# Kernel tuning notes

Measured on AMD Instinct MI355X. Metric: run time of the kernel, lower is better.

## Reference

```python
import jax, jax.numpy as jnp
import numpy as np

N_NODES = 100000
N_EDGES = 3200000
D_FEAT = 256
HIDDEN = 16


def setup_inputs() -> dict:
    key = jax.random.key(0)
    k1, k2, k3, k4 = jax.random.split(key, 4)
    x = jax.random.normal(k1, (N_NODES, D_FEAT), dtype=jnp.float32)
    edge_index = jax.random.randint(k2, (2, N_EDGES), 0, N_NODES, dtype=jnp.int64)
    # GCNConv linear weight (Glorot-ish scale) and bias
    W = jax.random.normal(k3, (D_FEAT, HIDDEN), dtype=jnp.float32) / np.sqrt(D_FEAT)
    b_conv = jnp.zeros((HIDDEN,), dtype=jnp.float32)
    W_fc = jax.random.normal(k4, (HIDDEN, 1), dtype=jnp.float32) / np.sqrt(HIDDEN)
    b_fc = jnp.zeros((1,), dtype=jnp.float32)
    return {"x": x, "edge_index": edge_index, "W": W, "b_conv": b_conv,
            "W_fc": W_fc, "b_fc": b_fc}


def reference(x, edge_index, W, b_conv, W_fc, b_fc):
    N = x.shape[0]
    # --- GCNConv: add self-loops, symmetric normalization, transform, scatter-add ---
    loop = jnp.arange(N, dtype=edge_index.dtype)
    src = jnp.concatenate([edge_index[0], loop])  # message sources (x_j)
    dst = jnp.concatenate([edge_index[1], loop])  # aggregation targets
    # degree of target nodes (edge weights = 1, self-loops included)
    deg = jax.ops.segment_sum(jnp.ones_like(dst, dtype=x.dtype), dst, num_segments=N)
    dinv = jnp.where(deg > 0, jax.lax.rsqrt(deg), 0.0)
    norm = dinv[src] * dinv[dst]  # [E+N]
    h = x @ W                       # [N, hidden] transform before propagation
    msg = h[src] * norm[:, None]    # gather + scale
    agg = jax.ops.segment_sum(msg, dst, num_segments=N)  # scatter-add
    out = agg + b_conv
    return out @ W_fc + b_fc
```

## Files before the change

kernel.cpp:

```cpp
#include <hip/hip_runtime.h>

#define DF 256
#define HID 16
#define WB 1024
#define PBITS 8
#define PMAX 512

__global__ void __launch_bounds__(256)
hist_kernel(const int* __restrict__ dst, unsigned* __restrict__ cntT, int P, int E, int Epw) {
    __shared__ unsigned h[PMAX];
    for (int i = threadIdx.x; i < P; i += 256) h[i] = 0u;
    __syncthreads();
    const int w = blockIdx.x;
    const size_t e0 = (size_t)w * Epw;
    long rem = (long)E - (long)e0;
    int m = rem < 0 ? 0 : (rem > Epw ? Epw : (int)rem);
    int i = threadIdx.x;
    for (; i + 768 < m; i += 1024) {
        unsigned d0 = (unsigned)dst[e0 + i];
        unsigned d1 = (unsigned)dst[e0 + i + 256];
        unsigned d2 = (unsigned)dst[e0 + i + 512];
        unsigned d3 = (unsigned)dst[e0 + i + 768];
        atomicAdd(&h[d0 >> PBITS], 1u); atomicAdd(&h[d1 >> PBITS], 1u);
        atomicAdd(&h[d2 >> PBITS], 1u); atomicAdd(&h[d3 >> PBITS], 1u);
    }
    for (; i < m; i += 256) atomicAdd(&h[((unsigned)dst[e0 + i]) >> PBITS], 1u);
    __syncthreads();
    for (int p = threadIdx.x; p < P; p += 256) cntT[(size_t)p * WB + w] = h[p];
}

__global__ void __launch_bounds__(1024)
rowscan_kernel(unsigned* __restrict__ cntT, unsigned* __restrict__ rowTotal) {
    __shared__ unsigned wsum[16];
    const int p = blockIdx.x, t = threadIdx.x, lane = t & 63, wv = t >> 6;
    unsigned v = cntT[(size_t)p * WB + t];
    unsigned xi = v;
#pragma unroll
    for (int off = 1; off < 64; off <<= 1) {
        unsigned u = __shfl_up(xi, off, 64);
        if (lane >= off) xi += u;
    }
    if (lane == 63) wsum[wv] = xi;
    __syncthreads();
    if (t < 16) {
        unsigned u = wsum[t];
#pragma unroll
        for (int off = 1; off < 16; off <<= 1) {
            unsigned uu = __shfl_up(u, off, 64);
            if (t >= off) u += uu;
        }
        wsum[t] = u;
    }
    __syncthreads();
    unsigned base = wv ? wsum[wv - 1] : 0u;
    cntT[(size_t)p * WB + t] = xi - v + base;
    if (t == 1023) rowTotal[p] = xi + base;
}

__global__ void __launch_bounds__(512)
partscan_kernel(const unsigned* __restrict__ rowTotal, unsigned* __restrict__ partBase,
                int P, int E) {
    __shared__ unsigned wsum[8];
    const int t = threadIdx.x, lane = t & 63, wv = t >> 6;
    unsigned v = (t < P) ? rowTotal[t] : 0u;
    unsigned xi = v;
#pragma unroll
    for (int off = 1; off < 64; off <<= 1) {
        unsigned u = __shfl_up(xi, off, 64);
        if (lane >= off) xi += u;
    }
    if (lane == 63) wsum[wv] = xi;
    __syncthreads();
    if (t < 8) {
        unsigned u = wsum[t];
#pragma unroll
        for (int off = 1; off < 8; off <<= 1) {
            unsigned uu = __shfl_up(u, off, 64);
            if (t >= off) u += uu;
        }
        wsum[t] = u;
    }
    __syncthreads();
    unsigned base = wv ? wsum[wv - 1] : 0u;
    if (t < P) partBase[t] = xi - v + base;
    if (t == 0) partBase[P] = (unsigned)E;
}

__global__ void __launch_bounds__(512)
binscatter_kernel(const int* __restrict__ src, const int* __restrict__ dst,
                  const unsigned* __restrict__ cntT, const unsigned* __restrict__ partBase,
                  unsigned* __restrict__ sorted, int P, int E, int Epw) {
    __shared__ unsigned cur[PMAX];
    const int w = blockIdx.x;
    for (int p = threadIdx.x; p < P; p += 512)
        cur[p] = partBase[p] + cntT[(size_t)p * WB + w];
    __syncthreads();
    const size_t e0 = (size_t)w * Epw;
    long rem = (long)E - (long)e0;
    int m = rem < 0 ? 0 : (rem > Epw ? Epw : (int)rem);
    int i = threadIdx.x;
    for (; i + 1536 < m; i += 2048) {
        unsigned s0 = (unsigned)src[e0 + i],        d0 = (unsigned)dst[e0 + i];
        unsigned s1 = (unsigned)src[e0 + i + 512],  d1 = (unsigned)dst[e0 + i + 512];
        unsigned s2 = (unsigned)src[e0 + i + 1024], d2 = (unsigned)dst[e0 + i + 1024];
        unsigned s3 = (unsigned)src[e0 + i + 1536], d3 = (unsigned)dst[e0 + i + 1536];
        unsigned t0 = atomicAdd(&cur[d0 >> PBITS], 1u);
        unsigned t1 = atomicAdd(&cur[d1 >> PBITS], 1u);
        unsigned t2 = atomicAdd(&cur[d2 >> PBITS], 1u);
        unsigned t3 = atomicAdd(&cur[d3 >> PBITS], 1u);
        sorted[t0] = (s0 << PBITS) | (d0 & 255u);
        sorted[t1] = (s1 << PBITS) | (d1 & 255u);
        sorted[t2] = (s2 << PBITS) | (d2 & 255u);
        sorted[t3] = (s3 << PBITS) | (d3 & 255u);
    }
    for (; i < m; i += 512) {
        unsigned s = (unsigned)src[e0 + i], d = (unsigned)dst[e0 + i];
        unsigned slot = atomicAdd(&cur[d >> PBITS], 1u);
        sorted[slot] = (s << PBITS) | (d & 255u);
    }
}

__global__ void __launch_bounds__(1024)
degfin_sval_kernel(const float* __restrict__ x, const unsigned* __restrict__ sorted,
                   const unsigned* __restrict__ partBase, const float* __restrict__ Wm,
                   const float* __restrict__ W_fc, float* __restrict__ dinv,
                   float* __restrict__ tval, int N) {
    __shared__ unsigned dc[256];
    __shared__ float sly[256];
    const int p = blockIdx.x, t = threadIdx.x;
    if (t < 256) dc[t] = 0u;
    __syncthreads();
    const unsigned b0 = partBase[p], b1 = partBase[p + 1];
    unsigned j = b0 + t;
    for (; j + 3072 < b1; j += 4096) {
        unsigned e0 = sorted[j], e1 = sorted[j + 1024], e2 = sorted[j + 2048], e3 = sorted[j + 3072];
        atomicAdd(&dc[e0 & 255u], 1u); atomicAdd(&dc[e1 & 255u], 1u);
        atomicAdd(&dc[e2 & 255u], 1u); atomicAdd(&dc[e3 & 255u], 1u);
    }
    for (; j < b1; j += 1024) atomicAdd(&dc[sorted[j] & 255u], 1u);
    {
        const int lane = t & 63, wv = t >> 6;
        float a0 = 0.f, a1 = 0.f, a2 = 0.f, a3 = 0.f;
        const float* wrow = Wm + (size_t)(lane * 4) * HID;
#pragma unroll
        for (int k = 0; k < HID; ++k) {
            float f = W_fc[k];
            a0 += wrow[k] * f;
            a1 += wrow[HID + k] * f;
            a2 += wrow[2 * HID + k] * f;
            a3 += wrow[3 * HID + k] * f;
        }
        for (int k = 0; k < 8; ++k) {
            int ra = wv + 16 * k, rb = ra + 128;
            int ia = (p << PBITS) + ra, ib = (p << PBITS) + rb;
            float sa = 0.f, sb = 0.f;
            if (ia < N) {
                float4 xa = reinterpret_cast<const float4*>(x + (size_t)ia * DF)[lane];
                sa = xa.x * a0 + xa.y * a1 + xa.z * a2 + xa.w * a3;
            }
            if (ib < N) {
                float4 xb = reinterpret_cast<const float4*>(x + (size_t)ib * DF)[lane];
                sb = xb.x * a0 + xb.y * a1 + xb.z * a2 + xb.w * a3;
            }
#pragma unroll
            for (int off = 32; off > 0; off >>= 1) {
                sa += __shfl_xor(sa, off, 64);
                sb += __shfl_xor(sb, off, 64);
            }
            if (lane == 0) { sly[ra] = sa; sly[rb] = sb; }
        }
    }
    __syncthreads();
    if (t < 256) {
        int i = (p << PBITS) + t;
        if (i < N) {
            float deg = 1.0f + (float)dc[t];
            float di = rsqrtf(deg);
            dinv[i] = di;
            tval[i] = sly[t] * di;
        }
    }
}

__global__ void __launch_bounds__(1024)
reduce_kernel(const unsigned* __restrict__ sorted, const unsigned* __restrict__ partBase,
              const float* __restrict__ tval, const float* __restrict__ dinv,
              const float* __restrict__ b_conv, const float* __restrict__ W_fc,
              const float* __restrict__ b_fc, float* __restrict__ out, int N) {
    __shared__ float facc[256];
    const int p = blockIdx.x, t = threadIdx.x;
    if (t < 256) facc[t] = 0.f;
    __syncthreads();
    const unsigned b0 = partBase[p], b1 = partBase[p + 1];
    unsigned j = b0 + t;
    for (; j + 3072 < b1; j += 4096) {
        unsigned e0 = sorted[j], e1 = sorted[j + 1024], e2 = sorted[j + 2048], e3 = sorted[j + 3072];
        float v0 = tval[e0 >> PBITS], v1 = tval[e1 >> PBITS];
        float v2 = tval[e2 >> PBITS], v3 = tval[e3 >> PBITS];
        atomicAdd(&facc[e0 & 255u], v0); atomicAdd(&facc[e1 & 255u], v1);
        atomicAdd(&facc[e2 & 255u], v2); atomicAdd(&facc[e3 & 255u], v3);
    }
    for (; j < b1; j += 1024) {
        unsigned e = sorted[j];
        atomicAdd(&facc[e & 255u], tval[e >> PBITS]);
    }
    __syncthreads();
    if (t < 256) {
        int i = (p << PBITS) + t;
        if (i < N) {
            float c = 0.f;
#pragma unroll
            for (int k = 0; k < HID; ++k) c += b_conv[k] * W_fc[k];
            float di = dinv[i];
            out[i] = di * (tval[i] + facc[t]) + c + b_fc[0];
        }
    }
}

__global__ void fb_sval(const float* __restrict__ x, const float* __restrict__ Wm,
                        const float* __restrict__ W_fc, float* __restrict__ sv, int N) {
    __shared__ float wl[DF];
    int k = threadIdx.x;
    float a = 0.f;
#pragma unroll
    for (int j = 0; j < HID; ++j) a += Wm[k * HID + j] * W_fc[j];
    wl[k] = a;
    __syncthreads();
    int lane = threadIdx.x & 63, wid = threadIdx.x >> 6;
    float4 wv = reinterpret_cast<const float4*>(wl)[lane];
    for (int row = blockIdx.x * 4 + wid; row < N; row += gridDim.x * 4) {
        float4 xv = reinterpret_cast<const float4*>(x + (size_t)row * DF)[lane];
        float acc = xv.x * wv.x + xv.y * wv.y + xv.z * wv.z + xv.w * wv.w;
#pragma unroll
        for (int off = 32; off > 0; off >>= 1) acc += __shfl_xor(acc, off, 64);
        if (lane == 0) sv[row] = acc;
    }
}
__global__ void fb_count(const int* __restrict__ dst, unsigned* __restrict__ cnt, int E) {
    int stride = gridDim.x * blockDim.x;
    for (int e = blockIdx.x * blockDim.x + threadIdx.x; e < E; e += stride)
        atomicAdd(&cnt[dst[e]], 1u);
}
__global__ void fb_node(const unsigned* __restrict__ cnt, const float* __restrict__ sv,
                        const float* __restrict__ b_conv, const float* __restrict__ W_fc,
                        const float* __restrict__ b_fc, float* __restrict__ dinv,
                        float* __restrict__ tval, float* __restrict__ out, int N) {
    int i = blockIdx.x * blockDim.x + threadIdx.x;
    if (i < N) {
        float c = 0.f;
#pragma unroll
        for (int j = 0; j < HID; ++j) c += b_conv[j] * W_fc[j];
        float deg = 1.0f + (float)cnt[i];
        float di = rsqrtf(deg);
        float s = sv[i];
        dinv[i] = di; tval[i] = s * di;
        out[i] = s / deg + c + b_fc[0];
    }
}
__global__ void fb_scatter(const int* __restrict__ src, const int* __restrict__ dst,
                           const float* __restrict__ tval, const float* __restrict__ dinv,
                           float* __restrict__ out, int E) {
    int stride = gridDim.x * blockDim.x;
    for (int e = blockIdx.x * blockDim.x + threadIdx.x; e < E; e += stride) {
        int si = src[e], di = dst[e];
        atomicAdd(&out[di], tval[si] * dinv[di]);
    }
}

extern "C" void kernel_launch(void* const* d_in, const int* in_sizes, int n_in,
                              void* d_out, int out_size, void* d_ws, size_t ws_size,
                              hipStream_t stream) {
    const float* x      = (const float*)d_in[0];
    const int*   ei     = (const int*)d_in[1];
    const float* Wm     = (const float*)d_in[2];
    const float* b_conv = (const float*)d_in[3];
    const float* W_fc   = (const float*)d_in[4];
    const float* b_fc   = (const float*)d_in[5];
    float* out = (float*)d_out;

    const int N = in_sizes[0] / DF;
    const int E = in_sizes[1] / 2;
    const int* src = ei;
    const int* dst = ei + E;

    const int P   = (N + 255) >> PBITS;
    const int Epw = (E + WB - 1) / WB;

    char* ws = (char*)d_ws;
    float* dinv = (float*)ws;
    float* tval = dinv + N;
    unsigned* cntT     = (unsigned*)(tval + N);
    unsigned* rowTotal = cntT + (size_t)P * WB;
    unsigned* partBase = rowTotal + 512;
    unsigned* sorted   = partBase + 520;

    const size_t need = ((size_t)2 * N + (size_t)P * WB + 512 + 520 + (size_t)E) * 4;

    if (P >= 1 && P <= PMAX && N <= (1 << 23) && ws_size >= need) {
        hist_kernel<<<WB, 256, 0, stream>>>(dst, cntT, P, E, Epw);
        rowscan_kernel<<<P, 1024, 0, stream>>>(cntT, rowTotal);
        partscan_kernel<<<1, 512, 0, stream>>>(rowTotal, partBase, P, E);
        binscatter_kernel<<<WB, 512, 0, stream>>>(src, dst, cntT, partBase, sorted, P, E, Epw);
        degfin_sval_kernel<<<P, 1024, 0, stream>>>(x, sorted, partBase, Wm, W_fc, dinv, tval, N);
        reduce_kernel<<<P, 1024, 0, stream>>>(sorted, partBase, tval, dinv,
                                              b_conv, W_fc, b_fc, out, N);
    } else {
        float* sv = tval + N;
        unsigned* fcnt = (unsigned*)(sv + N);
        hipMemsetAsync(fcnt, 0, (size_t)N * 4, stream);
        fb_sval<<<2048, 256, 0, stream>>>(x, Wm, W_fc, sv, N);
        fb_count<<<2048, 256, 0, stream>>>(dst, fcnt, E);
        fb_node<<<(N + 255) / 256, 256, 0, stream>>>(fcnt, sv, b_conv, W_fc, b_fc, dinv, tval, out, N);
        fb_scatter<<<2048, 256, 0, stream>>>(src, dst, tval, dinv, out, E);
    }
}
```

Baseline: 101.0 us.

## Fuse x-projection into histogram kernel and halve edge-chunk block count

Moves the per-node projection of x onto W·W_fc out of the degree-finalize kernel and into the histogram kernel, which processes rows in a grid-stride loop with four rows in flight per wave. The histogram block count drops from 1024 to 512 with 512 threads each, and the count matrix is stored block-major with padding, so the row scan now reads it strided. The aim is to overlap the large x read with the light histogram pass and to spread it across the whole grid instead of one block per partition. The cost is an extra N-float buffer for sv and a strided access pattern in the scan.

```diff
diff --git a/kernel.cpp b/kernel.cpp
--- a/kernel.cpp
+++ b/kernel.cpp
@@ -2,38 +2,84 @@
 
 #define DF 256
 #define HID 16
-#define WB 1024
+#define WB 512
 #define PBITS 8
 #define PMAX 512
-
-__global__ void __launch_bounds__(256)
-hist_kernel(const int* __restrict__ dst, unsigned* __restrict__ cntT, int P, int E, int Epw) {
+#define PPAD 512
+
+__global__ void __launch_bounds__(512)
+hist_sval_kernel(const float* __restrict__ x, const int* __restrict__ dst,
+                 const float* __restrict__ Wm, const float* __restrict__ W_fc,
+                 unsigned* __restrict__ cntS, float* __restrict__ sv,
+                 int N, int E, int P, int Epw) {
     __shared__ unsigned h[PMAX];
-    for (int i = threadIdx.x; i < P; i += 256) h[i] = 0u;
+    for (int i = threadIdx.x; i < P; i += 512) h[i] = 0u;
     __syncthreads();
     const int w = blockIdx.x;
     const size_t e0 = (size_t)w * Epw;
     long rem = (long)E - (long)e0;
     int m = rem < 0 ? 0 : (rem > Epw ? Epw : (int)rem);
     int i = threadIdx.x;
-    for (; i + 768 < m; i += 1024) {
+    for (; i + 1536 < m; i += 2048) {
         unsigned d0 = (unsigned)dst[e0 + i];
-        unsigned d1 = (unsigned)dst[e0 + i + 256];
-        unsigned d2 = (unsigned)dst[e0 + i + 512];
-        unsigned d3 = (unsigned)dst[e0 + i + 768];
+        unsigned d1 = (unsigned)dst[e0 + i + 512];
+        unsigned d2 = (unsigned)dst[e0 + i + 1024];
+        unsigned d3 = (unsigned)dst[e0 + i + 1536];
         atomicAdd(&h[d0 >> PBITS], 1u); atomicAdd(&h[d1 >> PBITS], 1u);
         atomicAdd(&h[d2 >> PBITS], 1u); atomicAdd(&h[d3 >> PBITS], 1u);
     }
-    for (; i < m; i += 256) atomicAdd(&h[((unsigned)dst[e0 + i]) >> PBITS], 1u);
-    __syncthreads();
-    for (int p = threadIdx.x; p < P; p += 256) cntT[(size_t)p * WB + w] = h[p];
-}
-
-__global__ void __launch_bounds__(1024)
-rowscan_kernel(unsigned* __restrict__ cntT, unsigned* __restrict__ rowTotal) {
-    __shared__ unsigned wsum[16];
-    const int p = blockIdx.x, t = threadIdx.x, lane = t & 63, wv = t >> 6;
-    unsigned v = cntT[(size_t)p * WB + t];
+    for (; i < m; i += 512) atomicAdd(&h[((unsigned)dst[e0 + i]) >> PBITS], 1u);
+    __syncthreads();
+    for (int p = threadIdx.x; p < P; p += 512) cntS[(size_t)w * PPAD + p] = h[p];
+
+    const int lane = threadIdx.x & 63, wid = threadIdx.x >> 6;
+    const int gw = w * 8 + wid;
+    const int GW = WB * 8;
+    float a0 = 0.f, a1 = 0.f, a2 = 0.f, a3 = 0.f;
+    {
+        const float* wrow = Wm + (size_t)(lane * 4) * HID;
+#pragma unroll
+        for (int k = 0; k < HID; ++k) {
+            float f = W_fc[k];
+            a0 += wrow[k] * f;
+            a1 += wrow[HID + k] * f;
+            a2 += wrow[2 * HID + k] * f;
+            a3 += wrow[3 * HID + k] * f;
+        }
+    }
+    for (int r0 = gw; r0 < N; r0 += 4 * GW) {
+        int r1 = r0 + GW, r2 = r0 + 2 * GW, r3 = r0 + 3 * GW;
+        float4 v0, v1, v2, v3;
+        v0 = reinterpret_cast<const float4*>(x + (size_t)r0 * DF)[lane];
+        if (r1 < N) v1 = reinterpret_cast<const float4*>(x + (size_t)r1 * DF)[lane];
+        if (r2 < N) v2 = reinterpret_cast<const float4*>(x + (size_t)r2 * DF)[lane];
+        if (r3 < N) v3 = reinterpret_cast<const float4*>(x + (size_t)r3 * DF)[lane];
+        float s0 = v0.x * a0 + v0.y * a1 + v0.z * a2 + v0.w * a3;
+        float s1 = (r1 < N) ? (v1.x * a0 + v1.y * a1 + v1.z * a2 + v1.w * a3) : 0.f;
+        float s2 = (r2 < N) ? (v2.x * a0 + v2.y * a1 + v2.z * a2 + v2.w * a3) : 0.f;
+        float s3 = (r3 < N) ? (v3.x * a0 + v3.y * a1 + v3.z * a2 + v3.w * a3) : 0.f;
+#pragma unroll
+        for (int off = 32; off > 0; off >>= 1) {
+            s0 += __shfl_xor(s0, off, 64);
+            s1 += __shfl_xor(s1, off, 64);
+            s2 += __shfl_xor(s2, off, 64);
+            s3 += __shfl_xor(s3, off, 64);
+        }
+        if (lane == 0) {
+            sv[r0] = s0;
+            if (r1 < N) sv[r1] = s1;
+            if (r2 < N) sv[r2] = s2;
+            if (r3 < N) sv[r3] = s3;
+        }
+    }
+}
+
+__global__ void __launch_bounds__(WB)
+rowscan_kernel(unsigned* __restrict__ cntS, unsigned* __restrict__ rowTotal) {
+    __shared__ unsigned wsum[8];
+    const int p = blockIdx.x, t = threadIdx.x;
+    const int lane = t & 63, wv = t >> 6;
+    unsigned v = cntS[(size_t)t * PPAD + p];
     unsigned xi = v;
 #pragma unroll
     for (int off = 1; off < 64; off <<= 1) {
@@ -42,10 +88,10 @@
     }
     if (lane == 63) wsum[wv] = xi;
     __syncthreads();
-    if (t < 16) {
+    if (t < 8) {
         unsigned u = wsum[t];
 #pragma unroll
-        for (int off = 1; off < 16; off <<= 1) {
+        for (int off = 1; off < 8; off <<= 1) {
             unsigned uu = __shfl_up(u, off, 64);
             if (t >= off) u += uu;
         }
@@ -53,8 +99,8 @@
     }
     __syncthreads();
     unsigned base = wv ? wsum[wv - 1] : 0u;
-    cntT[(size_t)p * WB + t] = xi - v + base;
-    if (t == 1023) rowTotal[p] = xi + base;
+    cntS[(size_t)t * PPAD + p] = xi - v + base;
+    if (t == 0) rowTotal[p] = wsum[7];
 }
 
 __global__ void __launch_bounds__(512)
@@ -88,12 +134,12 @@
 
 __global__ void __launch_bounds__(512)
 binscatter_kernel(const int* __restrict__ src, const int* __restrict__ dst,
-                  const unsigned* __restrict__ cntT, const unsigned* __restrict__ partBase,
+                  const unsigned* __restrict__ cntS, const unsigned* __restrict__ partBase,
                   unsigned* __restrict__ sorted, int P, int E, int Epw) {
     __shared__ unsigned cur[PMAX];
     const int w = blockIdx.x;
     for (int p = threadIdx.x; p < P; p += 512)
-        cur[p] = partBase[p] + cntT[(size_t)p * WB + w];
+        cur[p] = partBase[p] + cntS[(size_t)w * PPAD + p];
     __syncthreads();
     const size_t e0 = (size_t)w * Epw;
     long rem = (long)E - (long)e0;
@@ -121,12 +167,10 @@
 }
 
 __global__ void __launch_bounds__(1024)
-degfin_sval_kernel(const float* __restrict__ x, const unsigned* __restrict__ sorted,
-                   const unsigned* __restrict__ partBase, const float* __restrict__ Wm,
-                   const float* __restrict__ W_fc, float* __restrict__ dinv,
-                   float* __restrict__ tval, int N) {
+degfin_kernel(const unsigned* __restrict__ sorted, const unsigned* __restrict__ partBase,
+              const float* __restrict__ sv, float* __restrict__ dinv,
+              float* __restrict__ tval, int N) {
     __shared__ unsigned dc[256];
-    __shared__ float sly[256];
     const int p = blockIdx.x, t = threadIdx.x;
     if (t < 256) dc[t] = 0u;
     __syncthreads();
@@ -138,38 +182,6 @@
         atomicAdd(&dc[e2 & 255u], 1u); atomicAdd(&dc[e3 & 255u], 1u);
     }
     for (; j < b1; j += 1024) atomicAdd(&dc[sorted[j] & 255u], 1u);
-    {
-        const int lane = t & 63, wv = t >> 6;
-        float a0 = 0.f, a1 = 0.f, a2 = 0.f, a3 = 0.f;
-        const float* wrow = Wm + (size_t)(lane * 4) * HID;
-#pragma unroll
-        for (int k = 0; k < HID; ++k) {
-            float f = W_fc[k];
-            a0 += wrow[k] * f;
-            a1 += wrow[HID + k] * f;
-            a2 += wrow[2 * HID + k] * f;
-            a3 += wrow[3 * HID + k] * f;
-        }
-        for (int k = 0; k < 8; ++k) {
-            int ra = wv + 16 * k, rb = ra + 128;
-            int ia = (p << PBITS) + ra, ib = (p << PBITS) + rb;
-            float sa = 0.f, sb = 0.f;
-            if (ia < N) {
-                float4 xa = reinterpret_cast<const float4*>(x + (size_t)ia * DF)[lane];
-                sa = xa.x * a0 + xa.y * a1 + xa.z * a2 + xa.w * a3;
-            }
-            if (ib < N) {
-                float4 xb = reinterpret_cast<const float4*>(x + (size_t)ib * DF)[lane];
-                sb = xb.x * a0 + xb.y * a1 + xb.z * a2 + xb.w * a3;
-            }
-#pragma unroll
-            for (int off = 32; off > 0; off >>= 1) {
-                sa += __shfl_xor(sa, off, 64);
-                sb += __shfl_xor(sb, off, 64);
-            }
-            if (lane == 0) { sly[ra] = sa; sly[rb] = sb; }
-        }
-    }
     __syncthreads();
     if (t < 256) {
         int i = (p << PBITS) + t;
@@ -177,7 +189,7 @@
             float deg = 1.0f + (float)dc[t];
             float di = rsqrtf(deg);
             dinv[i] = di;
-            tval[i] = sly[t] * di;
+            tval[i] = sv[i] * di;
         }
     }
 }
@@ -287,26 +299,26 @@
     const int Epw = (E + WB - 1) / WB;
 
     char* ws = (char*)d_ws;
-    float* dinv = (float*)ws;
+    float* sv   = (float*)ws;
+    float* dinv = sv + N;
     float* tval = dinv + N;
-    unsigned* cntT     = (unsigned*)(tval + N);
-    unsigned* rowTotal = cntT + (size_t)P * WB;
+    unsigned* cntS     = (unsigned*)(tval + N);
+    unsigned* rowTotal = cntS + (size_t)WB * PPAD;
     unsigned* partBase = rowTotal + 512;
     unsigned* sorted   = partBase + 520;
 
-    const size_t need = ((size_t)2 * N + (size_t)P * WB + 512 + 520 + (size_t)E) * 4;
+    const size_t need = ((size_t)3 * N + (size_t)WB * PPAD + 512 + 520 + (size_t)E) * 4;
 
     if (P >= 1 && P <= PMAX && N <= (1 << 23) && ws_size >= need) {
-        hist_kernel<<<WB, 256, 0, stream>>>(dst, cntT, P, E, Epw);
-        rowscan_kernel<<<P, 1024, 0, stream>>>(cntT, rowTotal);
+        hist_sval_kernel<<<WB, 512, 0, stream>>>(x, dst, Wm, W_fc, cntS, sv, N, E, P, Epw);
+        rowscan_kernel<<<P, WB, 0, stream>>>(cntS, rowTotal);
         partscan_kernel<<<1, 512, 0, stream>>>(rowTotal, partBase, P, E);
-        binscatter_kernel<<<WB, 512, 0, stream>>>(src, dst, cntT, partBase, sorted, P, E, Epw);
-        degfin_sval_kernel<<<P, 1024, 0, stream>>>(x, sorted, partBase, Wm, W_fc, dinv, tval, N);
+        binscatter_kernel<<<WB, 512, 0, stream>>>(src, dst, cntS, partBase, sorted, P, E, Epw);
+        degfin_kernel<<<P, 1024, 0, stream>>>(sorted, partBase, sv, dinv, tval, N);
         reduce_kernel<<<P, 1024, 0, stream>>>(sorted, partBase, tval, dinv,
                                               b_conv, W_fc, b_fc, out, N);
     } else {
-        float* sv = tval + N;
-        unsigned* fcnt = (unsigned*)(sv + N);
+        unsigned* fcnt = (unsigned*)(tval + N);
         hipMemsetAsync(fcnt, 0, (size_t)N * 4, stream);
         fb_sval<<<2048, 256, 0, stream>>>(x, Wm, W_fc, sv, N);
         fb_count<<<2048, 256, 0, stream>>>(dst, fcnt, E);
```

New measurement: 84.97 us. 1.19x faster.
